# Performance work log

Measured on AMD Instinct MI355X. Metric: run time of the kernel, lower is better.

Reference implementation:

```python
import jax, jax.numpy as jnp
import numpy as np

B, N, F = 2, 2048, 512
W = 128          # winlen
D = 512          # d_model


def setup_inputs() -> dict:
    key = jax.random.key(0)
    k1, k2 = jax.random.split(key)
    x = jax.random.normal(k1, (B, N, F), dtype=jnp.float32)
    # Linear(in_features, 3*d_model, bias=False): weight shape (3D, F)
    W_lin = jax.random.normal(k2, (3 * D, F), dtype=jnp.float32) * 0.02
    return {"x": x, "W_lin": W_lin}


def reference(x, W_lin):
    b, n, f = x.shape
    qkv = jnp.einsum("bnf,ef->bne", x, W_lin)           # [B,N,3D]
    q, k, v = jnp.split(qkv, 3, axis=-1)                  # each [B,N,D]
    # Causal sliding window: position n sees [n-W+1, n], zero-padded on left.
    pad = W - 1
    k_pad = jnp.pad(k, ((0, 0), (pad, 0), (0, 0)))        # [B,N+W-1,D]
    v_pad = jnp.pad(v, ((0, 0), (pad, 0), (0, 0)))
    idx = jnp.arange(n)[:, None] + jnp.arange(W)[None, :]  # [N,W] -> k_pad[n+w]
    kr = k_pad[:, idx, :]                                  # [B,N,W,D]
    vr = v_pad[:, idx, :]                                  # [B,N,W,D]
    # NOTE: original forward does NOT apply attn_scale -> no scaling here.
    logits = jnp.einsum("bnd,bnwd->bnw", q, kr)           # [B,N,W]
    attn = jax.nn.softmax(logits, axis=-1)
    out = jnp.einsum("bnw,bnwd->bnd", attn, vr)           # [B,N,D]
    return out
```

## Files before the change

### kernel.cpp

```cpp
#include <hip/hip_runtime.h>
#include <cstdint>
#include <cstddef>

typedef unsigned short u16;
typedef unsigned int u32;
typedef u16 u16x4 __attribute__((ext_vector_type(4)));
typedef u16 u16x8 __attribute__((ext_vector_type(8)));
typedef u32 u32x2 __attribute__((ext_vector_type(2)));
typedef u32 u32x4 __attribute__((ext_vector_type(4)));
typedef _Float16 f16x8 __attribute__((ext_vector_type(8)));
typedef float f32x4 __attribute__((ext_vector_type(4)));

#define B_   2
#define N_   2048
#define F_   512
#define D_   512
#define W_   128
#define E3   1536
#define MTOT 4096
#define XELEMS (MTOT * F_)
#define WELEMS (E3 * F_)
#define QK_ELEMS (MTOT * D_)

__device__ __forceinline__ u16 f2h(float f) {
  return __builtin_bit_cast(u16, (_Float16)f);
}
__device__ __forceinline__ u32 pk2h(float a, float b) {
  return __builtin_bit_cast(u32, __builtin_amdgcn_cvt_pkrtz(a, b));
}
__device__ __forceinline__ f32x4 mfma_f16(u16x8 a, u16x8 b, f32x4 c) {
  return __builtin_amdgcn_mfma_f32_16x16x32_f16(
      __builtin_bit_cast(f16x8, a), __builtin_bit_cast(f16x8, b), c, 0, 0, 0);
}
__device__ __forceinline__ void glds16(const u16* g, u16* l) {
  __builtin_amdgcn_global_load_lds(
      (const __attribute__((address_space(1))) void*)g,
      (__attribute__((address_space(3))) void*)l, 16, 0, 0);
}

__global__ __launch_bounds__(256) void cvt_f16(const float* __restrict__ X,
                                               const float* __restrict__ Wl,
                                               u16* __restrict__ Xf, u16* __restrict__ Wf) {
  const int i = blockIdx.x * 256 + threadIdx.x;
  const int n4X = XELEMS / 4;
  if (i < n4X) {
    float4 v = ((const float4*)X)[i];
    ((u32x2*)Xf)[i] = (u32x2){pk2h(v.x, v.y), pk2h(v.z, v.w)};
  } else {
    int j = i - n4X;
    float4 v = ((const float4*)Wl)[j];
    ((u32x2*)Wf)[j] = (u32x2){pk2h(v.x, v.y), pk2h(v.z, v.w)};
  }
}

#define TM 128
#define TE 128
#define BK 32

__global__ __launch_bounds__(256) void qkv_gemm(const u16* __restrict__ Xf,
                                                const u16* __restrict__ Wf,
                                                u16* __restrict__ Qf,
                                                u16* __restrict__ Kf,
                                                u16* __restrict__ Vt) {
  __shared__ __align__(16) u16 smem[16896];
  u16* sA = smem;
  u16* sB = smem + 4096;

  const int tid = threadIdx.x;
  const int m0 = blockIdx.x * TM;
  const int e0 = blockIdx.y * TE;
  const int lane = tid & 63;
  const int wave = tid >> 6;
  const int wm = (wave >> 1) * 64;
  const int we = (wave & 1) * 64;
  const int qd = lane >> 4;
  const int l16 = lane & 15;

  const int lrow = lane >> 2;
  const int cg = (lane & 3) ^ ((lrow >> 1) & 3);
  const int lkc = cg * 8;

  f32x4 acc[4][4];
#pragma unroll
  for (int i = 0; i < 4; ++i)
#pragma unroll
    for (int j = 0; j < 4; ++j) acc[i][j] = (f32x4){0.f, 0.f, 0.f, 0.f};

  const int r0 = wave * 32;
  const size_t ga0 = (size_t)(m0 + r0 + lrow) * F_ + lkc;
  const size_t ga1 = (size_t)(m0 + r0 + 16 + lrow) * F_ + lkc;
  const size_t gb0 = (size_t)(e0 + r0 + lrow) * F_ + lkc;
  const size_t gb1 = (size_t)(e0 + r0 + 16 + lrow) * F_ + lkc;
  u16* lA0 = sA + r0 * 32;
  u16* lA1 = sA + (r0 + 16) * 32;
  u16* lB0 = sB + r0 * 32;
  u16* lB1 = sB + (r0 + 16) * 32;

  const int swz = (l16 >> 1) & 3;
  const int rdoff = (qd ^ swz) * 8;

  for (int k0 = 0; k0 < F_; k0 += BK) {
    glds16(Xf + ga0 + k0, lA0);
    glds16(Xf + ga1 + k0, lA1);
    glds16(Wf + gb0 + k0, lB0);
    glds16(Wf + gb1 + k0, lB1);
    __syncthreads();

    u16x8 fA[4], fB[4];
#pragma unroll
    for (int mi = 0; mi < 4; ++mi)
      fA[mi] = *(const u16x8*)&sA[(wm + mi * 16 + l16) * 32 + rdoff];
#pragma unroll
    for (int ei = 0; ei < 4; ++ei)
      fB[ei] = *(const u16x8*)&sB[(we + ei * 16 + l16) * 32 + rdoff];
#pragma unroll
    for (int mi = 0; mi < 4; ++mi)
#pragma unroll
      for (int ei = 0; ei < 4; ++ei)
        acc[mi][ei] = mfma_f16(fA[mi], fB[ei], acc[mi][ei]);
    __syncthreads();
  }

  const int third = e0 >> 9;
  if (third < 2) {
    u16* P = third ? Kf : Qf;
    const int ecol0 = (e0 & 511) + we;
    const int odd = l16 & 1;
#pragma unroll
    for (int mi = 0; mi < 4; ++mi)
#pragma unroll
      for (int ei = 0; ei < 4; ++ei) {
        float x0 = acc[mi][ei][0], x1 = acc[mi][ei][1];
        float x2 = acc[mi][ei][2], x3 = acc[mi][ei][3];
        float t0 = __shfl_xor(x0, 1), t1 = __shfl_xor(x1, 1);
        float t2 = __shfl_xor(x2, 1), t3 = __shfl_xor(x3, 1);
        u32 pa = odd ? pk2h(t2, x2) : pk2h(x0, t0);
        u32 pb = odd ? pk2h(t3, x3) : pk2h(x1, t1);
        int mrow = m0 + wm + mi * 16 + qd * 4 + odd * 2;
        int colp = ecol0 + ei * 16 + (l16 & ~1);
        *(u32*)(P + (size_t)mrow * D_ + colp) = pa;
        *(u32*)(P + (size_t)(mrow + 1) * D_ + colp) = pb;
      }
  } else {
    u16* vbuf = smem + wave * 4224;
#pragma unroll
    for (int mi = 0; mi < 4; ++mi)
#pragma unroll
      for (int ei = 0; ei < 4; ++ei)
#pragma unroll
        for (int r2 = 0; r2 < 2; ++r2) {
          int e_in = ei * 16 + l16;
          int m_in = mi * 16 + qd * 4 + r2 * 2;
          u32 p = pk2h(acc[mi][ei][r2 * 2], acc[mi][ei][r2 * 2 + 1]);
          *(u32*)&vbuf[e_in * 66 + m_in] = p;
        }
    __builtin_amdgcn_s_waitcnt(0);
    const int dbase = (e0 - 1024) + we;
    const int mb = (m0 & 2047) + wm;
    const int bb = m0 >> 11;
    u16* vt = Vt + (size_t)bb * (D_ * N_);
#pragma unroll
    for (int it = 0; it < 4; ++it) {
      int e_in = it * 16 + (lane >> 2);
      int mc = lane & 3;
      u32 q0[8];
#pragma unroll
      for (int c4 = 0; c4 < 8; ++c4)
        q0[c4] = *(const u32*)&vbuf[e_in * 66 + mc * 16 + c4 * 2];
      u16* gp = vt + (size_t)(dbase + e_in) * N_ + mb + mc * 16;
      *(u32x4*)gp = (u32x4){q0[0], q0[1], q0[2], q0[3]};
      *(u32x4*)(gp + 8) = (u32x4){q0[4], q0[5], q0[6], q0[7]};
    }
  }
}

#define TQA 16
#define SA 200
#define SP 208

__global__ __launch_bounds__(512) void attn_kernel(const u16* __restrict__ Qf,
                                                   const u16* __restrict__ Kf,
                                                   const u16* __restrict__ Vt,
                                                   float* __restrict__ Out) {
  const int m0 = blockIdx.x * TQA;
  const int b = m0 >> 11;
  const int n0 = m0 & 2047;
  const int t = threadIdx.x;
  const int lane = t & 63;
  const int w = t >> 6;
  const int qd = lane >> 4;
  const int l16 = lane & 15;

  __shared__ __align__(16) float att[2][TQA][SA];
  __shared__ __align__(16) u16 pS[TQA][SP];

  const int jw = w & 3;
  const int kh = w >> 2;

  f32x4 acc[3];
#pragma unroll
  for (int nt = 0; nt < 3; ++nt) acc[nt] = (f32x4){0.f, 0.f, 0.f, 0.f};

  const size_t qrow = (size_t)(m0 + l16) * D_ + qd * 8;
  for (int ks = kh * 8; ks < kh * 8 + 8; ++ks) {
    u16x8 qv = *(const u16x8*)(Qf + qrow + ks * 32);
#pragma unroll
    for (int nt = 0; nt < 3; ++nt) {
      int j = (jw * 3 + nt) * 16 + l16;
      int rl = n0 - 128 + j;
      int rg = b * N_ + (rl > 0 ? rl : 0);
      u16x8 kv = *(const u16x8*)(Kf + (size_t)rg * D_ + ks * 32 + qd * 8);
      acc[nt] = mfma_f16(qv, kv, acc[nt]);
    }
  }
#pragma unroll
  for (int nt = 0; nt < 3; ++nt)
#pragma unroll
    for (int r = 0; r < 4; ++r)
      att[kh][qd * 4 + r][(jw * 3 + nt) * 16 + l16] = acc[nt][r];
  __syncthreads();

  {
    const int i = t >> 5;
    const int c = t & 31;
    float ev[6];
    float mx = -1e30f;
#pragma unroll
    for (int s = 0; s < 6; ++s) {
      int j = c * 6 + s;
      bool inw = (j >= i + 1) && (j <= i + 128);
      float v = -1e30f;
      if (inw) v = (n0 - 128 + j < 0) ? 0.f : att[0][i][j] + att[1][i][j];
      ev[s] = v;
      mx = fmaxf(mx, v);
    }
    mx = fmaxf(mx, __shfl_xor(mx, 1));
    mx = fmaxf(mx, __shfl_xor(mx, 2));
    mx = fmaxf(mx, __shfl_xor(mx, 4));
    mx = fmaxf(mx, __shfl_xor(mx, 8));
    mx = fmaxf(mx, __shfl_xor(mx, 16));
    float sum = 0.f;
#pragma unroll
    for (int s = 0; s < 6; ++s) {
      ev[s] = (ev[s] > -1e29f) ? __expf(ev[s] - mx) : 0.f;
      sum += ev[s];
    }
    sum += __shfl_xor(sum, 1);
    sum += __shfl_xor(sum, 2);
    sum += __shfl_xor(sum, 4);
    sum += __shfl_xor(sum, 8);
    sum += __shfl_xor(sum, 16);
    const float inv = 1.f / sum;
#pragma unroll
    for (int s = 0; s < 6; ++s) {
      int j = c * 6 + s;
      bool zv = (n0 - 128 + j) < 0;
      pS[i][j] = zv ? (u16)0 : f2h(ev[s] * inv);
    }
  }
  __syncthreads();

  f32x4 oacc[4];
#pragma unroll
  for (int nt = 0; nt < 4; ++nt) oacc[nt] = (f32x4){0.f, 0.f, 0.f, 0.f};

  const u16* vtb = Vt + (size_t)b * (D_ * N_);
  for (int kk = 0; kk < 6; ++kk) {
    u16x8 pa = *(const u16x8*)&pS[l16][kk * 32 + qd * 8];
    const int rl = n0 - 128 + kk * 32 + qd * 8;
#pragma unroll
    for (int nt = 0; nt < 4; ++nt) {
      int d = w * 64 + nt * 16 + l16;
      u16x8 vv = *(const u16x8*)(vtb + (size_t)d * N_ + rl);
      oacc[nt] = mfma_f16(pa, vv, oacc[nt]);
    }
  }
#pragma unroll
  for (int nt = 0; nt < 4; ++nt)
#pragma unroll
    for (int r = 0; r < 4; ++r)
      Out[(size_t)(m0 + qd * 4 + r) * D_ + w * 64 + nt * 16 + l16] = oacc[nt][r];
}

extern "C" void kernel_launch(void* const* d_in, const int* in_sizes, int n_in,
                              void* d_out, int out_size, void* d_ws, size_t ws_size,
                              hipStream_t stream) {
  const float* x = (const float*)d_in[0];
  const float* wl = (const float*)d_in[1];
  float* out = (float*)d_out;

  u16* Xf = (u16*)d_ws;
  u16* Wf = Xf + XELEMS;
  u16* Qf = Wf + WELEMS;
  u16* Kf = Qf + QK_ELEMS;
  u16* Vt = Kf + QK_ELEMS;

  cvt_f16<<<(XELEMS + WELEMS) / 4 / 256, 256, 0, stream>>>(x, wl, Xf, Wf);
  dim3 g1(MTOT / TM, E3 / TE);
  qkv_gemm<<<g1, 256, 0, stream>>>(Xf, Wf, Qf, Kf, Vt);
  attn_kernel<<<MTOT / TQA, 512, 0, stream>>>(Qf, Kf, Vt, out);
}
```

Baseline: 96.56 us.

## Double GEMM K-tile to 64 with new swizzle; trim unused attention key tiles

The QKV GEMM now stages 64-wide K slices per iteration, using a new XOR swizzle over 8 column groups. This halves the number of barrier-synchronised loop iterations and issues more MFMAs per sync. In the attention kernel, the last wave group computes only one 16-column key tile instead of three, and the PV loop drops its sixth 32-column chunk. Those tiles fall outside the 144-wide window a 16-query tile can need. This saves score MFMAs, K/V loads and LDS writes, but it depends on the softmax never reading the skipped columns. It also doubles the shared memory used per stage.

```diff
diff --git a/kernel.cpp b/kernel.cpp
--- a/kernel.cpp
+++ b/kernel.cpp
@@ -55,7 +55,7 @@
 
 #define TM 128
 #define TE 128
-#define BK 32
+#define BK 64
 
 __global__ __launch_bounds__(256) void qkv_gemm(const u16* __restrict__ Xf,
                                                 const u16* __restrict__ Wf,
@@ -64,7 +64,7 @@
                                                 u16* __restrict__ Vt) {
   __shared__ __align__(16) u16 smem[16896];
   u16* sA = smem;
-  u16* sB = smem + 4096;
+  u16* sB = smem + 8192;
 
   const int tid = threadIdx.x;
   const int m0 = blockIdx.x * TM;
@@ -76,9 +76,9 @@
   const int qd = lane >> 4;
   const int l16 = lane & 15;
 
-  const int lrow = lane >> 2;
-  const int cg = (lane & 3) ^ ((lrow >> 1) & 3);
-  const int lkc = cg * 8;
+  const int lrow8 = lane >> 3;
+  const int c8 = lane & 7;
+  const int sk = (c8 ^ lrow8) * 8;
 
   f32x4 acc[4][4];
 #pragma unroll
@@ -87,37 +87,42 @@
     for (int j = 0; j < 4; ++j) acc[i][j] = (f32x4){0.f, 0.f, 0.f, 0.f};
 
   const int r0 = wave * 32;
-  const size_t ga0 = (size_t)(m0 + r0 + lrow) * F_ + lkc;
-  const size_t ga1 = (size_t)(m0 + r0 + 16 + lrow) * F_ + lkc;
-  const size_t gb0 = (size_t)(e0 + r0 + lrow) * F_ + lkc;
-  const size_t gb1 = (size_t)(e0 + r0 + 16 + lrow) * F_ + lkc;
-  u16* lA0 = sA + r0 * 32;
-  u16* lA1 = sA + (r0 + 16) * 32;
-  u16* lB0 = sB + r0 * 32;
-  u16* lB1 = sB + (r0 + 16) * 32;
-
-  const int swz = (l16 >> 1) & 3;
-  const int rdoff = (qd ^ swz) * 8;
+  size_t gA[4], gB[4];
+  u16 *lA[4], *lB[4];
+#pragma unroll
+  for (int t = 0; t < 4; ++t) {
+    gA[t] = (size_t)(m0 + r0 + 8 * t + lrow8) * F_ + sk;
+    gB[t] = (size_t)(e0 + r0 + 8 * t + lrow8) * F_ + sk;
+    lA[t] = sA + (r0 + 8 * t) * 64;
+    lB[t] = sB + (r0 + 8 * t) * 64;
+  }
+
+  const int xk = l16 & 7;
 
   for (int k0 = 0; k0 < F_; k0 += BK) {
-    glds16(Xf + ga0 + k0, lA0);
-    glds16(Xf + ga1 + k0, lA1);
-    glds16(Wf + gb0 + k0, lB0);
-    glds16(Wf + gb1 + k0, lB1);
+#pragma unroll
+    for (int t = 0; t < 4; ++t) glds16(Xf + gA[t] + k0, lA[t]);
+#pragma unroll
+    for (int t = 0; t < 4; ++t) glds16(Wf + gB[t] + k0, lB[t]);
     __syncthreads();
 
-    u16x8 fA[4], fB[4];
-#pragma unroll
-    for (int mi = 0; mi < 4; ++mi)
-      fA[mi] = *(const u16x8*)&sA[(wm + mi * 16 + l16) * 32 + rdoff];
-#pragma unroll
-    for (int ei = 0; ei < 4; ++ei)
-      fB[ei] = *(const u16x8*)&sB[(we + ei * 16 + l16) * 32 + rdoff];
-#pragma unroll
-    for (int mi = 0; mi < 4; ++mi)
+#pragma unroll
+    for (int ks = 0; ks < 2; ++ks) {
+      u16x8 fA[4], fB[4];
+#pragma unroll
+      for (int mi = 0; mi < 4; ++mi)
+        fA[mi] = *(const u16x8*)&sA[(wm + mi * 16 + l16) * 64 +
+                                    (((ks * 4 + qd) ^ xk) * 8)];
 #pragma unroll
       for (int ei = 0; ei < 4; ++ei)
-        acc[mi][ei] = mfma_f16(fA[mi], fB[ei], acc[mi][ei]);
+        fB[ei] = *(const u16x8*)&sB[(we + ei * 16 + l16) * 64 +
+                                    (((ks * 4 + qd) ^ xk) * 8)];
+#pragma unroll
+      for (int mi = 0; mi < 4; ++mi)
+#pragma unroll
+        for (int ei = 0; ei < 4; ++ei)
+          acc[mi][ei] = mfma_f16(fA[mi], fB[ei], acc[mi][ei]);
+    }
     __syncthreads();
   }
 
@@ -196,6 +201,7 @@
 
   const int jw = w & 3;
   const int kh = w >> 2;
+  const int ntm = (jw < 3) ? 3 : 1;
 
   f32x4 acc[3];
 #pragma unroll
@@ -206,18 +212,22 @@
     u16x8 qv = *(const u16x8*)(Qf + qrow + ks * 32);
 #pragma unroll
     for (int nt = 0; nt < 3; ++nt) {
-      int j = (jw * 3 + nt) * 16 + l16;
-      int rl = n0 - 128 + j;
-      int rg = b * N_ + (rl > 0 ? rl : 0);
-      u16x8 kv = *(const u16x8*)(Kf + (size_t)rg * D_ + ks * 32 + qd * 8);
-      acc[nt] = mfma_f16(qv, kv, acc[nt]);
+      if (nt < ntm) {
+        int j = (jw * 3 + nt) * 16 + l16;
+        int rl = n0 - 128 + j;
+        int rg = b * N_ + (rl > 0 ? rl : 0);
+        u16x8 kv = *(const u16x8*)(Kf + (size_t)rg * D_ + ks * 32 + qd * 8);
+        acc[nt] = mfma_f16(qv, kv, acc[nt]);
+      }
     }
   }
 #pragma unroll
   for (int nt = 0; nt < 3; ++nt)
-#pragma unroll
-    for (int r = 0; r < 4; ++r)
-      att[kh][qd * 4 + r][(jw * 3 + nt) * 16 + l16] = acc[nt][r];
+    if (nt < ntm) {
+#pragma unroll
+      for (int r = 0; r < 4; ++r)
+        att[kh][qd * 4 + r][(jw * 3 + nt) * 16 + l16] = acc[nt][r];
+    }
   __syncthreads();
 
   {
@@ -265,7 +275,7 @@
   for (int nt = 0; nt < 4; ++nt) oacc[nt] = (f32x4){0.f, 0.f, 0.f, 0.f};
 
   const u16* vtb = Vt + (size_t)b * (D_ * N_);
-  for (int kk = 0; kk < 6; ++kk) {
+  for (int kk = 0; kk < 5; ++kk) {
     u16x8 pa = *(const u16x8*)&pS[l16][kk * 32 + qd * 8];
     const int rl = n0 - 128 + kk * 32 + qd * 8;
 #pragma unroll
```

Measured after the change: 96.47 us. About the same (-0.1%).

## Fuse fp32-to-fp16 conversion into QKV GEMM with register-prefetched double buffering

Applied to the files above, without the earlier changes.

Removes the separate cvt_f16 kernel. The GEMM now loads fp32 X and W directly, converts them to fp16 in registers and stores them into double-buffered LDS, prefetching the next K-slice while the MFMAs run. This saves a launch and the fp16 round-trip through global memory, at the cost of twice the global load bytes per tile and extra VGPR pressure. The attention kernel also skips key tiles and PV steps that fall entirely outside the causal window (the 4th jw group does one tile instead of three, and the PV loop runs 5 steps instead of 6).

```diff
diff --git a/kernel.cpp b/kernel.cpp
--- a/kernel.cpp
+++ b/kernel.cpp
@@ -18,8 +18,6 @@
 #define W_   128
 #define E3   1536
 #define MTOT 4096
-#define XELEMS (MTOT * F_)
-#define WELEMS (E3 * F_)
 #define QK_ELEMS (MTOT * D_)
 
 __device__ __forceinline__ u16 f2h(float f) {
@@ -32,39 +30,18 @@
   return __builtin_amdgcn_mfma_f32_16x16x32_f16(
       __builtin_bit_cast(f16x8, a), __builtin_bit_cast(f16x8, b), c, 0, 0, 0);
 }
-__device__ __forceinline__ void glds16(const u16* g, u16* l) {
-  __builtin_amdgcn_global_load_lds(
-      (const __attribute__((address_space(1))) void*)g,
-      (__attribute__((address_space(3))) void*)l, 16, 0, 0);
-}
-
-__global__ __launch_bounds__(256) void cvt_f16(const float* __restrict__ X,
-                                               const float* __restrict__ Wl,
-                                               u16* __restrict__ Xf, u16* __restrict__ Wf) {
-  const int i = blockIdx.x * 256 + threadIdx.x;
-  const int n4X = XELEMS / 4;
-  if (i < n4X) {
-    float4 v = ((const float4*)X)[i];
-    ((u32x2*)Xf)[i] = (u32x2){pk2h(v.x, v.y), pk2h(v.z, v.w)};
-  } else {
-    int j = i - n4X;
-    float4 v = ((const float4*)Wl)[j];
-    ((u32x2*)Wf)[j] = (u32x2){pk2h(v.x, v.y), pk2h(v.z, v.w)};
-  }
-}
 
 #define TM 128
 #define TE 128
 #define BK 32
-
-__global__ __launch_bounds__(256) void qkv_gemm(const u16* __restrict__ Xf,
-                                                const u16* __restrict__ Wf,
+#define NK (F_ / BK)
+
+__global__ __launch_bounds__(256) void qkv_gemm(const float* __restrict__ X,
+                                                const float* __restrict__ Wl,
                                                 u16* __restrict__ Qf,
                                                 u16* __restrict__ Kf,
                                                 u16* __restrict__ Vt) {
   __shared__ __align__(16) u16 smem[16896];
-  u16* sA = smem;
-  u16* sB = smem + 4096;
 
   const int tid = threadIdx.x;
   const int m0 = blockIdx.x * TM;
@@ -76,49 +53,91 @@
   const int qd = lane >> 4;
   const int l16 = lane & 15;
 
-  const int lrow = lane >> 2;
-  const int cg = (lane & 3) ^ ((lrow >> 1) & 3);
-  const int lkc = cg * 8;
+  const int r0 = wave * 32;
+  const int sr = lane >> 2;
+  const int sc = lane & 3;
+  const int key = (sr >> 1) & 3;
+  const int cl = sc ^ key;
+  const int la = (r0 + sr) * 32 + cl * 8;
+
+  const float* ga = X + (size_t)(m0 + r0 + sr) * F_ + sc * 8;
+  const float* gb = Wl + (size_t)(e0 + r0 + sr) * F_ + sc * 8;
 
   f32x4 acc[4][4];
 #pragma unroll
   for (int i = 0; i < 4; ++i)
 #pragma unroll
     for (int j = 0; j < 4; ++j) acc[i][j] = (f32x4){0.f, 0.f, 0.f, 0.f};
-
-  const int r0 = wave * 32;
-  const size_t ga0 = (size_t)(m0 + r0 + lrow) * F_ + lkc;
-  const size_t ga1 = (size_t)(m0 + r0 + 16 + lrow) * F_ + lkc;
-  const size_t gb0 = (size_t)(e0 + r0 + lrow) * F_ + lkc;
-  const size_t gb1 = (size_t)(e0 + r0 + 16 + lrow) * F_ + lkc;
-  u16* lA0 = sA + r0 * 32;
-  u16* lA1 = sA + (r0 + 16) * 32;
-  u16* lB0 = sB + r0 * 32;
-  u16* lB1 = sB + (r0 + 16) * 32;
 
   const int swz = (l16 >> 1) & 3;
   const int rdoff = (qd ^ swz) * 8;
 
-  for (int k0 = 0; k0 < F_; k0 += BK) {
-    glds16(Xf + ga0 + k0, lA0);
-    glds16(Xf + ga1 + k0, lA1);
-    glds16(Wf + gb0 + k0, lB0);
-    glds16(Wf + gb1 + k0, lB1);
+  {
+    float4 a0 = *(const float4*)(ga);
+    float4 a1 = *(const float4*)(ga + 4);
+    float4 a2 = *(const float4*)(ga + 16 * F_);
+    float4 a3 = *(const float4*)(ga + 16 * F_ + 4);
+    float4 b0 = *(const float4*)(gb);
+    float4 b1 = *(const float4*)(gb + 4);
+    float4 b2 = *(const float4*)(gb + 16 * F_);
+    float4 b3 = *(const float4*)(gb + 16 * F_ + 4);
+    u16* sA = smem;
+    u16* sB = smem + 4096;
+    *(u32x4*)&sA[la] = (u32x4){pk2h(a0.x, a0.y), pk2h(a0.z, a0.w),
+                               pk2h(a1.x, a1.y), pk2h(a1.z, a1.w)};
+    *(u32x4*)&sA[la + 512] = (u32x4){pk2h(a2.x, a2.y), pk2h(a2.z, a2.w),
+                                     pk2h(a3.x, a3.y), pk2h(a3.z, a3.w)};
+    *(u32x4*)&sB[la] = (u32x4){pk2h(b0.x, b0.y), pk2h(b0.z, b0.w),
+                               pk2h(b1.x, b1.y), pk2h(b1.z, b1.w)};
+    *(u32x4*)&sB[la + 512] = (u32x4){pk2h(b2.x, b2.y), pk2h(b2.z, b2.w),
+                                     pk2h(b3.x, b3.y), pk2h(b3.z, b3.w)};
+  }
+
+  for (int k = 0; k < NK; ++k) {
+    u16* sAk = smem + (k & 1) * 8192;
+    u16* sBk = sAk + 4096;
     __syncthreads();
 
     u16x8 fA[4], fB[4];
 #pragma unroll
     for (int mi = 0; mi < 4; ++mi)
-      fA[mi] = *(const u16x8*)&sA[(wm + mi * 16 + l16) * 32 + rdoff];
+      fA[mi] = *(const u16x8*)&sAk[(wm + mi * 16 + l16) * 32 + rdoff];
 #pragma unroll
     for (int ei = 0; ei < 4; ++ei)
-      fB[ei] = *(const u16x8*)&sB[(we + ei * 16 + l16) * 32 + rdoff];
+      fB[ei] = *(const u16x8*)&sBk[(we + ei * 16 + l16) * 32 + rdoff];
+
+    float4 a0, a1, a2, a3, b0, b1, b2, b3;
+    if (k + 1 < NK) {
+      const float* gan = ga + (k + 1) * BK;
+      const float* gbn = gb + (k + 1) * BK;
+      a0 = *(const float4*)(gan);
+      a1 = *(const float4*)(gan + 4);
+      a2 = *(const float4*)(gan + 16 * F_);
+      a3 = *(const float4*)(gan + 16 * F_ + 4);
+      b0 = *(const float4*)(gbn);
+      b1 = *(const float4*)(gbn + 4);
+      b2 = *(const float4*)(gbn + 16 * F_);
+      b3 = *(const float4*)(gbn + 16 * F_ + 4);
+    }
+
 #pragma unroll
     for (int mi = 0; mi < 4; ++mi)
 #pragma unroll
       for (int ei = 0; ei < 4; ++ei)
         acc[mi][ei] = mfma_f16(fA[mi], fB[ei], acc[mi][ei]);
-    __syncthreads();
+
+    if (k + 1 < NK) {
+      u16* nA = smem + ((k + 1) & 1) * 8192;
+      u16* nB = nA + 4096;
+      *(u32x4*)&nA[la] = (u32x4){pk2h(a0.x, a0.y), pk2h(a0.z, a0.w),
+                                 pk2h(a1.x, a1.y), pk2h(a1.z, a1.w)};
+      *(u32x4*)&nA[la + 512] = (u32x4){pk2h(a2.x, a2.y), pk2h(a2.z, a2.w),
+                                       pk2h(a3.x, a3.y), pk2h(a3.z, a3.w)};
+      *(u32x4*)&nB[la] = (u32x4){pk2h(b0.x, b0.y), pk2h(b0.z, b0.w),
+                                 pk2h(b1.x, b1.y), pk2h(b1.z, b1.w)};
+      *(u32x4*)&nB[la + 512] = (u32x4){pk2h(b2.x, b2.y), pk2h(b2.z, b2.w),
+                                       pk2h(b3.x, b3.y), pk2h(b3.z, b3.w)};
+    }
   }
 
   const int third = e0 >> 9;
@@ -142,6 +161,7 @@
         *(u32*)(P + (size_t)(mrow + 1) * D_ + colp) = pb;
       }
   } else {
+    __syncthreads();
     u16* vbuf = smem + wave * 4224;
 #pragma unroll
     for (int mi = 0; mi < 4; ++mi)
@@ -196,6 +216,7 @@
 
   const int jw = w & 3;
   const int kh = w >> 2;
+  const int ntm = (jw < 3) ? 3 : 1;
 
   f32x4 acc[3];
 #pragma unroll
@@ -206,18 +227,22 @@
     u16x8 qv = *(const u16x8*)(Qf + qrow + ks * 32);
 #pragma unroll
     for (int nt = 0; nt < 3; ++nt) {
-      int j = (jw * 3 + nt) * 16 + l16;
-      int rl = n0 - 128 + j;
-      int rg = b * N_ + (rl > 0 ? rl : 0);
-      u16x8 kv = *(const u16x8*)(Kf + (size_t)rg * D_ + ks * 32 + qd * 8);
-      acc[nt] = mfma_f16(qv, kv, acc[nt]);
+      if (nt < ntm) {
+        int j = (jw * 3 + nt) * 16 + l16;
+        int rl = n0 - 128 + j;
+        int rg = b * N_ + (rl > 0 ? rl : 0);
+        u16x8 kv = *(const u16x8*)(Kf + (size_t)rg * D_ + ks * 32 + qd * 8);
+        acc[nt] = mfma_f16(qv, kv, acc[nt]);
+      }
     }
   }
 #pragma unroll
   for (int nt = 0; nt < 3; ++nt)
-#pragma unroll
-    for (int r = 0; r < 4; ++r)
-      att[kh][qd * 4 + r][(jw * 3 + nt) * 16 + l16] = acc[nt][r];
+    if (nt < ntm) {
+#pragma unroll
+      for (int r = 0; r < 4; ++r)
+        att[kh][qd * 4 + r][(jw * 3 + nt) * 16 + l16] = acc[nt][r];
+    }
   __syncthreads();
 
   {
@@ -265,7 +290,7 @@
   for (int nt = 0; nt < 4; ++nt) oacc[nt] = (f32x4){0.f, 0.f, 0.f, 0.f};
 
   const u16* vtb = Vt + (size_t)b * (D_ * N_);
-  for (int kk = 0; kk < 6; ++kk) {
+  for (int kk = 0; kk < 5; ++kk) {
     u16x8 pa = *(const u16x8*)&pS[l16][kk * 32 + qd * 8];
     const int rl = n0 - 128 + kk * 32 + qd * 8;
 #pragma unroll
@@ -289,14 +314,11 @@
   const float* wl = (const float*)d_in[1];
   float* out = (float*)d_out;
 
-  u16* Xf = (u16*)d_ws;
-  u16* Wf = Xf + XELEMS;
-  u16* Qf = Wf + WELEMS;
+  u16* Qf = (u16*)d_ws;
   u16* Kf = Qf + QK_ELEMS;
   u16* Vt = Kf + QK_ELEMS;
 
-  cvt_f16<<<(XELEMS + WELEMS) / 4 / 256, 256, 0, stream>>>(x, wl, Xf, Wf);
   dim3 g1(MTOT / TM, E3 / TE);
-  qkv_gemm<<<g1, 256, 0, stream>>>(Xf, Wf, Qf, Kf, Vt);
+  qkv_gemm<<<g1, 256, 0, stream>>>(x, wl, Qf, Kf, Vt);
   attn_kernel<<<MTOT / TQA, 512, 0, stream>>>(Qf, Kf, Vt, out);
 }
```

Result: faster. 94.49 us (-2.1%).
